# Performance work log

Hardware: AMD Instinct MI355X
Metric: run time of the kernel (lower is better)

The kernel has to match this reference:

```python
import jax, jax.numpy as jnp
import numpy as np

SEQ, B, OBS, H = 128, 256, 64, 1024

def setup_inputs() -> dict:
    key = jax.random.key(0)
    ks = jax.random.split(key, 16)
    s = 0.03  # keep weights small so tanh/sigmoid stay in a sane range
    n = lambda k, shape, sc=s: jax.random.normal(k, shape, jnp.float32) * sc
    return {
        "x": jax.random.normal(ks[0], (SEQ * B, OBS), jnp.float32),
        "done": jax.random.randint(ks[1], (SEQ * B,), 0, 2).astype(jnp.int32),
        "h0": n(ks[2], (2, B, H), 0.1),
        "c0": n(ks[3], (2, B, H), 0.1),
        "W_ih0": n(ks[4], (4 * H, OBS)),
        "W_hh0": n(ks[5], (4 * H, H)),
        "b_ih0": jnp.zeros((4 * H,), jnp.float32),
        "b_hh0": jnp.zeros((4 * H,), jnp.float32),
        "W_ih1": n(ks[6], (4 * H, H)),
        "W_hh1": n(ks[7], (4 * H, H)),
        "b_ih1": jnp.zeros((4 * H,), jnp.float32),
        "b_hh1": jnp.zeros((4 * H,), jnp.float32),
        "ln_g": jnp.ones((H,), jnp.float32),
        "ln_b": jnp.zeros((H,), jnp.float32),
        "W1": n(ks[8], (512, H)),
        "b1": jnp.zeros((512,), jnp.float32),
        "W2": n(ks[9], (128, 512)),
        "b2": jnp.zeros((128,), jnp.float32),
        "W3": n(ks[10], (64, 128)),
        "b3": jnp.zeros((64,), jnp.float32),
        "Wv": n(ks[11], (1, 64)),
        "bv": jnp.zeros((1,), jnp.float32),
    }

def _lstm_cell(xin, h, c, Wih, Whh, bih, bhh):
    # PyTorch gate order: input, forget, cell(g), output
    g = xin @ Wih.T + bih + h @ Whh.T + bhh
    i, f, gg, o = jnp.split(g, 4, axis=-1)
    c2 = jax.nn.sigmoid(f) * c + jax.nn.sigmoid(i) * jnp.tanh(gg)
    h2 = jax.nn.sigmoid(o) * jnp.tanh(c2)
    return h2, c2

def reference(x, done, h0, c0, W_ih0, W_hh0, b_ih0, b_hh0, W_ih1, W_hh1,
              b_ih1, b_hh1, ln_g, ln_b, W1, b1, W2, b2, W3, b3, Wv, bv):
    batch = h0.shape[1]
    obs = x.shape[-1]
    xs = x.reshape(-1, batch, obs)                      # (S, B, obs)
    ds = done.reshape(-1, batch).astype(x.dtype)        # (S, B)

    def step(carry, td):
        h, c = carry                                    # each (2, B, H)
        xt, dt = td
        m = (1.0 - dt)[:, None]                         # reset mask (B, 1)
        h0_, c0_ = _lstm_cell(xt, h[0] * m, c[0] * m, W_ih0, W_hh0, b_ih0, b_hh0)
        h1_, c1_ = _lstm_cell(h0_, h[1] * m, c[1] * m, W_ih1, W_hh1, b_ih1, b_hh1)
        return (jnp.stack([h0_, h1_]), jnp.stack([c0_, c1_])), h1_

    (hN, cN), hs = jax.lax.scan(step, (h0, c0), (xs, ds))
    hidden = hs.reshape(-1, hs.shape[-1])               # (S*B, H)

    # LayerNorm (eps = 1e-5, torch default)
    mu = hidden.mean(-1, keepdims=True)
    var = jnp.mean(jnp.square(hidden - mu), -1, keepdims=True)
    hn = (hidden - mu) * jax.lax.rsqrt(var + 1e-5) * ln_g + ln_b

    a = jax.nn.elu(hn @ W1.T + b1)
    a = jax.nn.elu(a @ W2.T + b2)
    a = jax.nn.elu(a @ W3.T + b3)
    value = a @ Wv.T + bv                               # (S*B, 1)
    return value, hN, cN
```

## Files before the change

### kernel.cpp

```cpp
#include <hip/hip_runtime.h>
#include <cstdint>
#include <cstddef>

typedef unsigned short u16;
typedef __attribute__((ext_vector_type(8))) short short8;
typedef __attribute__((ext_vector_type(4))) float f32x4;

#define SEQ 128
#define BATCH 256
#define HID 1024
#define LSZ 262144

#define MFMA(a,b,c) __builtin_amdgcn_mfma_f32_16x16x32_bf16((a),(b),(c),0,0,0)

#define GLDS_CG(g, l) __builtin_amdgcn_global_load_lds( \
  (__attribute__((address_space(1))) void*)(uintptr_t)(const void*)(g), \
  (__attribute__((address_space(3))) void*)(unsigned)(uintptr_t)(void*)(l), 16, 0, 17)
#define GLDS_NC(g, l) __builtin_amdgcn_global_load_lds( \
  (__attribute__((address_space(1))) void*)(uintptr_t)(const void*)(g), \
  (__attribute__((address_space(3))) void*)(unsigned)(uintptr_t)(void*)(l), 16, 0, 0)

__device__ __forceinline__ u16 f2b(float f) {
  union { float f; unsigned u; } v; v.f = f;
  unsigned r = (v.u + 0x7FFFu + ((v.u >> 16) & 1u)) >> 16;
  return (u16)r;
}
__device__ __forceinline__ float b2f(u16 h) {
  union { unsigned u; float f; } v; v.u = ((unsigned)h) << 16; return v.f;
}
__device__ __forceinline__ float sigm(float x){ return 1.f/(1.f + __expf(-x)); }
__device__ __forceinline__ float tanh_f(float x){
  x = fminf(15.f, fmaxf(-15.f, x));
  float e = __expf(2.f*x); return (e-1.f)/(e+1.f);
}
__device__ __forceinline__ float eluf(float x){ return x > 0.f ? x : expm1f(x); }

__device__ __forceinline__ void store_cg(u16* p, short8 v) {
  asm volatile("global_store_dwordx4 %0, %1, off sc0 sc1" :: "v"(p), "v"(v) : "memory");
}
__device__ __forceinline__ void wait_vm0() {
  asm volatile("s_waitcnt vmcnt(0)" ::: "memory");
}
__device__ __forceinline__ void waitgroup(int* f, int tgt) {
  if (threadIdx.x < 64) {
    int idx = threadIdx.x & 31;
    while (__hip_atomic_load(f + idx, __ATOMIC_RELAXED, __HIP_MEMORY_SCOPE_AGENT) < tgt)
      __builtin_amdgcn_s_sleep(1);
  }
  asm volatile("" ::: "memory");
  __builtin_amdgcn_s_barrier();
  __builtin_amdgcn_sched_barrier(0);
}

static const size_t OFF_W0F  = 0;
static const size_t OFF_W1F  = 8912896;
static const size_t OFF_XF   = 25690112;
static const size_t OFF_H0U  = 29884416;
static const size_t OFF_C0   = 30932992;
static const size_t OFF_C1   = 31981568;
static const size_t OFF_H1U  = 33030144;
static const size_t OFF_BS0  = 100663296;
static const size_t OFF_BS1  = 100679680;
static const size_t OFF_MU   = 100697088;
static const size_t OFF_RSTD = 100828160;
static const size_t OFF_W1LN = 100959232;
static const size_t OFF_S1   = 102007808;
static const size_t OFF_B1P  = 102009856;
static const size_t OFF_W2B  = 102011904;
static const size_t OFF_W3B  = 102142976;
static const size_t OFF_A1   = 102159360;
static const size_t OFF_A2   = 0;
static const size_t OFF_A3   = 8912896;
static const size_t OFF_H0M  = 102159360;
static const size_t OFF_H1M  = 102159360 + 1048576;

__global__ void prep_wf(const float* __restrict__ wih, const float* __restrict__ whh,
                        u16* __restrict__ out, int nkb, int kx) {
  int b = blockIdx.x; int cg = b >> 3, ct = b & 7;
  int g = ct >> 1;
  int n = nkb << 9;
  for (int e = threadIdx.x; e < n; e += 256) {
    int kb = e >> 9, r = e & 511;
    int q = r >> 7, col16 = (r >> 3) & 15, j = r & 7;
    int hl = (ct & 1) * 16 + col16;
    int gr = g * HID + cg * 32 + hl;
    int k = kb * 32 + q * 8 + j;
    float w = (k < kx) ? wih[(size_t)gr * kx + k] : whh[(size_t)gr * HID + (k - kx)];
    out[((size_t)(cg * nkb + kb) * 8 + ct) * 512 + r] = f2b(w);
  }
}

__global__ void prep_w1ln(const float* __restrict__ w1, const float* __restrict__ lng,
                          const float* __restrict__ lnb, const float* __restrict__ b1,
                          u16* __restrict__ w1ln, float* __restrict__ S1, float* __restrict__ b1p) {
  int j = blockIdx.x;
  float s = 0.f, bb = 0.f;
  for (int k = threadIdx.x; k < HID; k += 256) {
    float w = w1[(size_t)j * HID + k];
    u16 q = f2b(w * lng[k]);
    w1ln[(size_t)j * HID + k] = q;
    s += b2f(q);
    bb += w * lnb[k];
  }
  __shared__ float r1[256], r2[256];
  r1[threadIdx.x] = s; r2[threadIdx.x] = bb;
  __syncthreads();
  for (int o = 128; o > 0; o >>= 1) {
    if (threadIdx.x < (unsigned)o) { r1[threadIdx.x] += r1[threadIdx.x+o]; r2[threadIdx.x] += r2[threadIdx.x+o]; }
    __syncthreads();
  }
  if (threadIdx.x == 0) { S1[j] = r1[0]; b1p[j] = b1[j] + r2[0]; }
}

__global__ void prep_misc(const float* bih0, const float* bhh0, const float* bih1, const float* bhh1,
                          const float* x, const float* h0in, const float* c0in,
                          const float* w2, const float* w3, const int* done,
                          float* bs0, float* bs1, u16* xf, u16* h0m, u16* h1m,
                          float* c0buf, float* c1buf, u16* w2b, u16* w3b, int* flg) {
  size_t i = (size_t)blockIdx.x * blockDim.x + threadIdx.x;
  if (i < 4096) { bs0[i] = bih0[i] + bhh0[i]; return; }
  i -= 4096;
  if (i < 4096) { bs1[i] = bih1[i] + bhh1[i]; return; }
  i -= 4096;
  if (i < 2097152) {
    int o = (int)i;
    int r = o & 511, tile = o >> 9;
    int q = r >> 7, rl = (r >> 3) & 15, j = r & 7;
    int kb = tile & 1, v = tile >> 1;
    int grt = v & 15, t = v >> 4;
    int row = grt * 16 + rl, k = kb * 32 + q * 8 + j;
    xf[o] = f2b(x[((size_t)t * BATCH + row) * 64 + k]);
    return;
  }
  i -= 2097152;
  if (i < 262144) {
    int o = (int)i;
    int r = o & 511, tile = o >> 9;
    int q = r >> 7, rl = (r >> 3) & 15, j = r & 7;
    int grt = tile >> 5, kb = tile & 31;
    int row = grt * 16 + rl, h = kb * 32 + q * 8 + j;
    h0m[o] = done[row] ? (u16)0 : f2b(h0in[(size_t)row * HID + h]);
    return;
  }
  i -= 262144;
  if (i < 262144) {
    int o = (int)i;
    int r = o & 511, tile = o >> 9;
    int q = r >> 7, rl = (r >> 3) & 15, j = r & 7;
    int grt = tile >> 5, kb = tile & 31;
    int row = grt * 16 + rl, h = kb * 32 + q * 8 + j;
    h1m[o] = done[row] ? (u16)0 : f2b(h0in[LSZ + (size_t)row * HID + h]);
    return;
  }
  i -= 262144;
  if (i < LSZ) { c0buf[i] = c0in[i]; return; }
  i -= LSZ;
  if (i < LSZ) { c1buf[i] = c0in[LSZ + i]; return; }
  i -= LSZ;
  if (i < 65536) { w2b[i] = f2b(w2[i]); return; }
  i -= 65536;
  if (i < 8192) { w3b[i] = f2b(w3[i]); return; }
  i -= 8192;
  if (i < 512) { flg[i] = 0; return; }
}

__global__ __launch_bounds__(256, 2) void lstm_persist(
    const u16* __restrict__ w0f, const u16* __restrict__ w1f, const u16* __restrict__ xf,
    u16* __restrict__ h0u, u16* __restrict__ h1u,
    u16* __restrict__ h0m, u16* __restrict__ h1m,
    float* __restrict__ c0b, float* __restrict__ c1b,
    const float* __restrict__ bs0, const float* __restrict__ bs1,
    const int* __restrict__ done, int* __restrict__ flg,
    float* __restrict__ dout)
{
  const int bid = blockIdx.x;
  const int layer = bid >> 8;
  const int rg = (bid >> 5) & 7;
  const int cg = bid & 31;
  const int tid = threadIdx.x;
  const int lane = tid & 63, wv = tid >> 6;
  const int quad = lane >> 4, c16 = lane & 15;
  const int NKB = layer ? 64 : 34;
  const int NC  = layer ? 8 : 5;
  const u16* Wf = layer ? w1f : w0f;
  const float* bs = layer ? bs1 : bs0;
  float* cb = layer ? c1b : c0b;
  int* fl0 = flg;
  int* fl1 = flg + 256;
  int* myf = (layer ? fl1 : fl0) + rg * 32 + cg;
  int* g0 = fl0 + rg * 32;
  int* g1 = fl1 + rg * 32;

  __shared__ __align__(16) u16 smem[32768];
  float* gl = (float*)smem;

  const short8 z8 = {0,0,0,0,0,0,0,0};

  for (int t = 0; t < SEQ; ++t) {
    if (layer == 0) {
      if (t >= 1) waitgroup(g0, t);
    } else {
      waitgroup(g0, t + 1);
      if (t >= 1) waitgroup(g1, t);
    }

    auto issueA = [&](int p) {
      int oc = p; if (oc > NC - 1) oc = NC - 1;
      u16* lb = &smem[((unsigned)(p & 3)) * 8192];
      #pragma unroll
      for (int s = 0; s < 2; ++s) {
        int kbl = wv + s * 4;
        int kb = oc * 8 + kbl; if (kb > NKB - 1) kb = NKB - 1;
        u16* lt = lb + (unsigned)(kbl * 2) * 512;
        if (layer == 0) {
          if (kb < 2) {
            #pragma unroll
            for (int j = 0; j < 2; ++j) {
              const u16* g = xf + ((size_t)((t * 16 + rg * 2 + j) * 2 + kb)) * 512 + lane * 8;
              GLDS_NC(g, lt + j * 512);
            }
          } else {
            #pragma unroll
            for (int j = 0; j < 2; ++j) {
              const u16* g = h0m + (size_t)(t & 1) * 262144
                                 + (size_t)((rg * 2 + j) * 32 + (kb - 2)) * 512 + lane * 8;
              GLDS_CG(g, lt + j * 512);
            }
          }
        } else {
          if (kb < 32) {
            #pragma unroll
            for (int j = 0; j < 2; ++j) {
              const u16* g = h0u + (size_t)((t + 1) & 1) * 262144
                                 + (size_t)((rg * 2 + j) * 32 + kb) * 512 + lane * 8;
              GLDS_CG(g, lt + j * 512);
            }
          } else {
            #pragma unroll
            for (int j = 0; j < 2; ++j) {
              const u16* g = h1m + (size_t)(t & 1) * 262144
                                 + (size_t)((rg * 2 + j) * 32 + (kb - 32)) * 512 + lane * 8;
              GLDS_CG(g, lt + j * 512);
            }
          }
        }
      }
    };

    auto loadB = [&](int p, short8 (&vB)[8][2]) {
      int oc = p; if (oc > NC - 1) oc = NC - 1;
      #pragma unroll
      for (int kbl = 0; kbl < 8; ++kbl) {
        int kb = oc * 8 + kbl; if (kb > NKB - 1) kb = NKB - 1;
        #pragma unroll
        for (int h = 0; h < 2; ++h)
          vB[kbl][h] = *(const short8*)(Wf + ((size_t)(cg * NKB + kb) * 8 + wv * 2 + h) * 512 + lane * 8);
      }
    };

    f32x4 acc[2][2];
    #pragma unroll
    for (int a = 0; a < 2; ++a) { acc[a][0] = (f32x4){0,0,0,0}; acc[a][1] = (f32x4){0,0,0,0}; }

    auto comp = [&](int p, short8 (&vB)[8][2]) {
      int kbc = NKB - p * 8; if (kbc > 8) kbc = 8;
      const u16* sb = &smem[((unsigned)(p & 3)) * 8192] + lane * 8;
      #pragma unroll
      for (int kbl = 0; kbl < 8; ++kbl) if (kbl < kbc) {
        #pragma unroll
        for (int a = 0; a < 2; ++a) {
          short8 af = *(const short8*)(sb + (kbl * 2 + a) * 512);
          acc[a][0] = MFMA(af, vB[kbl][0], acc[a][0]);
          acc[a][1] = MFMA(af, vB[kbl][1], acc[a][1]);
        }
      }
    };

    short8 vB0[8][2], vB1[8][2];

    loadB(0, vB0);
    asm volatile("" ::: "memory");
    issueA(0);
    asm volatile("" ::: "memory");
    issueA(1);

#define CHUNK(CC, VBL, VBU) \
    loadB((CC) + 1, VBL); \
    asm volatile("" ::: "memory"); \
    issueA((CC) + 2); \
    asm volatile("s_waitcnt vmcnt(24)" ::: "memory"); \
    __builtin_amdgcn_s_barrier(); \
    __builtin_amdgcn_sched_barrier(0); \
    comp((CC), VBU);

    int c = 0;
    for (;;) {
      CHUNK(c, vB1, vB0) if (++c == NC) break;
      CHUNK(c, vB0, vB1) if (++c == NC) break;
    }
#undef CHUNK

    wait_vm0();
    __syncthreads();

    #pragma unroll
    for (int a = 0; a < 2; ++a)
      #pragma unroll
      for (int ct = 0; ct < 2; ++ct)
        #pragma unroll
        for (int rgi = 0; rgi < 4; ++rgi)
          gl[(a * 16 + quad * 4 + rgi) * 132 + wv * 32 + ct * 16 + c16] = acc[a][ct][rgi];
    __syncthreads();

    if (layer == 0 && t >= 2) waitgroup(g1, t - 1);

    if (tid < 128) {
      int row = tid >> 2;
      int q = tid & 3;
      int h8 = q * 8;
      int rowg = rg * 32 + row;
      int H0 = cg * 32 + h8;
      const float* glp = gl + row * 132;
      float m = done[t * BATCH + rowg] ? 0.f : 1.f;
      int nx = (t < SEQ - 1) ? done[(t + 1) * BATCH + rowg] : 0;
      float* cp = cb + (size_t)rowg * HID + H0;
      short8 hv;
      float h2a[8], c2a[8];
      #pragma unroll
      for (int j = 0; j < 8; ++j) {
        float ivv = glp[h8 + j]      + bs[H0 + j];
        float fvv = glp[32 + h8 + j] + bs[HID + H0 + j];
        float gvv = glp[64 + h8 + j] + bs[2*HID + H0 + j];
        float ovv = glp[96 + h8 + j] + bs[3*HID + H0 + j];
        float c2 = sigm(fvv) * (cp[j] * m) + sigm(ivv) * tanh_f(gvv);
        float h2 = sigm(ovv) * tanh_f(c2);
        cp[j] = c2;
        h2a[j] = h2; c2a[j] = c2;
        ((u16*)&hv)[j] = f2b(h2);
      }
      short8 hm = nx ? z8 : hv;
      size_t off = (size_t)((rg * 2 + (row >> 4)) * 32 + cg) * 512 + (size_t)(q * 16 + (row & 15)) * 8;
      if (layer == 0) {
        store_cg(h0u + (size_t)((t + 1) & 1) * 262144 + off, hv);
        if (t < SEQ - 1) store_cg(h0m + (size_t)((t + 1) & 1) * 262144 + off, hm);
      } else {
        store_cg(h1u + (size_t)(t + 1) * 262144 + off, hv);
        if (t < SEQ - 1) store_cg(h1m + (size_t)((t + 1) & 1) * 262144 + off, hm);
      }
      if (t == SEQ - 1) {
        float* dh = dout + 32768 + (size_t)layer * LSZ + (size_t)rowg * HID + H0;
        float* dc = dout + 32768 + 2 * LSZ + (size_t)layer * LSZ + (size_t)rowg * HID + H0;
        #pragma unroll
        for (int j = 0; j < 8; ++j) { dh[j] = h2a[j]; dc[j] = c2a[j]; }
      }
    }
    wait_vm0();
    __syncthreads();
    if (tid == 0) __hip_atomic_fetch_add(myf, 1, __ATOMIC_RELAXED, __HIP_MEMORY_SCOPE_AGENT);
  }
}

__global__ void ln_stats(const u16* __restrict__ h1u, float* __restrict__ mu, float* __restrict__ rstd) {
  int R = blockIdx.x * 4 + (threadIdx.x >> 6);
  int l = threadIdx.x & 63;
  int t = R >> 8, brow = R & 255, grt = brow >> 4, rl = brow & 15;
  const u16* base = h1u + (size_t)(t + 1) * 262144 + (size_t)(grt * 32 + (l >> 1)) * 512;
  int q2 = (l & 1) * 2;
  short8 v0 = *(const short8*)(base + (q2 * 16 + rl) * 8);
  short8 v1 = *(const short8*)(base + ((q2 + 1) * 16 + rl) * 8);
  float s = 0.f, q = 0.f;
  #pragma unroll
  for (int e = 0; e < 8; ++e) {
    float a = b2f((u16)v0[e]); s += a; q += a*a;
    float b = b2f((u16)v1[e]); s += b; q += b*b;
  }
  for (int o = 32; o > 0; o >>= 1) { s += __shfl_xor(s, o); q += __shfl_xor(q, o); }
  if (l == 0) {
    float mm = s * (1.f/1024.f);
    float var = q * (1.f/1024.f) - mm*mm;
    mu[R] = mm; rstd[R] = rsqrtf(var + 1e-5f);
  }
}

__global__ __launch_bounds__(512, 4) void mlp_gemm(
    const u16* __restrict__ A, int lda, int amode,
    const u16* __restrict__ B, int K, int N,
    u16* __restrict__ out, int ldo, int mode, int swiz,
    const float* __restrict__ mu, const float* __restrict__ rstd,
    const float* __restrict__ S1v, const float* __restrict__ bias)
{
  int nt, mtb;
  if (swiz) { int p = blockIdx.x * gridDim.y + blockIdx.y; nt = p & 3; mtb = p >> 2; }
  else { nt = blockIdx.x; mtb = blockIdx.y; }
  const int tid = threadIdx.x, lane = tid & 63, wv = tid >> 6;
  const int quad = lane >> 4, c16 = lane & 15;
  __shared__ __align__(16) u16 Am[16384], Bm[16384];
  f32x4 acc[8];
  #pragma unroll
  for (int i = 0; i < 8; ++i) acc[i] = (f32x4){0.f,0.f,0.f,0.f};

  int arow[4], akl[4], bcol[4];
  #pragma unroll
  for (int i = 0; i < 4; ++i) {
    int s = tid + i * 512, sub = s >> 6, lp = s & 63;
    int ks = sub >> 3, u = sub & 7;
    arow[i] = mtb * 128 + u * 16 + (lp & 15);
    akl[i]  = ks * 32 + (lp >> 4) * 8;
    bcol[i] = nt * 128 + u * 16 + (lp & 15);
  }
  short8 vA[4], vB[4];
  const short8 z8 = {0,0,0,0,0,0,0,0};
  const int NCH = K >> 7;
  auto load_stage = [&](int ci) {
    int kc = ci << 7;
    #pragma unroll
    for (int i = 0; i < 4; ++i) {
      if (amode) {
        int R = arow[i], k = kc + akl[i];
        const u16* p = A + (size_t)((R >> 8) + 1) * 262144
                         + (size_t)(((R >> 4) & 15) * 32 + (k >> 5)) * 512
                         + (size_t)((((k >> 3) & 3) * 16 + (R & 15)) * 8);
        vA[i] = *(const short8*)p;
      } else {
        vA[i] = *(const short8*)(A + (size_t)arow[i] * lda + kc + akl[i]);
      }
      vB[i] = (bcol[i] < N) ? *(const short8*)(B + (size_t)bcol[i] * K + kc + akl[i]) : z8;
    }
  };
  load_stage(0);
  for (int ci = 0; ci < NCH; ++ci) {
    #pragma unroll
    for (int i = 0; i < 4; ++i) {
      *(short8*)&Am[(size_t)(tid + i*512) * 8] = vA[i];
      *(short8*)&Bm[(size_t)(tid + i*512) * 8] = vB[i];
    }
    __syncthreads();
    if (ci + 1 < NCH) load_stage(ci + 1);
    #pragma unroll
    for (int ks = 0; ks < 4; ++ks) {
      short8 bf = *(const short8*)&Bm[((ks*8 + wv)*64 + lane) * 8];
      #pragma unroll
      for (int rt = 0; rt < 8; ++rt) {
        short8 af = *(const short8*)&Am[((ks*8 + rt)*64 + lane) * 8];
        acc[rt] = MFMA(af, bf, acc[rt]);
      }
    }
    __syncthreads();
  }
  int col = nt * 128 + wv * 16 + c16;
  if (col < N) {
    #pragma unroll
    for (int rt = 0; rt < 8; ++rt) {
      #pragma unroll
      for (int rgi = 0; rgi < 4; ++rgi) {
        int row = mtb * 128 + rt * 16 + quad * 4 + rgi;
        float v = acc[rt][rgi];
        if (mode == 0) v = v * rstd[row] - mu[row] * rstd[row] * S1v[col] + bias[col];
        else           v = v + bias[col];
        v = eluf(v);
        out[(size_t)row * ldo + col] = f2b(v);
      }
    }
  }
}

__global__ void value_head(const u16* __restrict__ a3, const float* __restrict__ wv,
                           const float* __restrict__ bv, float* __restrict__ dout) {
  int row = blockIdx.x * 256 + threadIdx.x;
  const short8* p = (const short8*)(a3 + (size_t)row * 64);
  float s = bv[0];
  #pragma unroll
  for (int j = 0; j < 8; ++j) {
    short8 v = p[j];
    #pragma unroll
    for (int e = 0; e < 8; ++e) s += b2f((u16)v[e]) * wv[j*8+e];
  }
  dout[row] = s;
}

extern "C" void kernel_launch(void* const* d_in, const int* in_sizes, int n_in,
                              void* d_out, int out_size, void* d_ws, size_t ws_size,
                              hipStream_t stream) {
  (void)in_sizes; (void)n_in; (void)out_size; (void)ws_size;
  const float* x    = (const float*)d_in[0];
  const int*   done = (const int*)d_in[1];
  const float* h0in = (const float*)d_in[2];
  const float* c0in = (const float*)d_in[3];
  const float* wih0 = (const float*)d_in[4];
  const float* whh0 = (const float*)d_in[5];
  const float* bih0 = (const float*)d_in[6];
  const float* bhh0 = (const float*)d_in[7];
  const float* wih1 = (const float*)d_in[8];
  const float* whh1 = (const float*)d_in[9];
  const float* bih1 = (const float*)d_in[10];
  const float* bhh1 = (const float*)d_in[11];
  const float* lng  = (const float*)d_in[12];
  const float* lnb  = (const float*)d_in[13];
  const float* w1   = (const float*)d_in[14];
  const float* b1   = (const float*)d_in[15];
  const float* w2   = (const float*)d_in[16];
  const float* b2   = (const float*)d_in[17];
  const float* w3   = (const float*)d_in[18];
  const float* b3   = (const float*)d_in[19];
  const float* wvp  = (const float*)d_in[20];
  const float* bvp  = (const float*)d_in[21];
  float* dout = (float*)d_out;
  char* ws = (char*)d_ws;

  u16*   w0f  = (u16*)(ws + OFF_W0F);
  u16*   w1f  = (u16*)(ws + OFF_W1F);
  u16*   xf   = (u16*)(ws + OFF_XF);
  u16*   h0u  = (u16*)(ws + OFF_H0U);
  u16*   h1u  = (u16*)(ws + OFF_H1U);
  u16*   h0m  = (u16*)(ws + OFF_H0M);
  u16*   h1m  = (u16*)(ws + OFF_H1M);
  float* c0b  = (float*)(ws + OFF_C0);
  float* c1b  = (float*)(ws + OFF_C1);
  float* bs0  = (float*)(ws + OFF_BS0);
  float* bs1  = (float*)(ws + OFF_BS1);
  int*   flg  = (int*)(ws + OFF_MU);
  float* mu   = (float*)(ws + OFF_MU);
  float* rstd = (float*)(ws + OFF_RSTD);
  u16*   w1ln = (u16*)(ws + OFF_W1LN);
  float* s1   = (float*)(ws + OFF_S1);
  float* b1p  = (float*)(ws + OFF_B1P);
  u16*   w2b  = (u16*)(ws + OFF_W2B);
  u16*   w3b  = (u16*)(ws + OFF_W3B);
  u16*   a1   = (u16*)(ws + OFF_A1);
  u16*   a2   = (u16*)(ws + OFF_A2);
  u16*   a3   = (u16*)(ws + OFF_A3);

  prep_wf<<<256, 256, 0, stream>>>(wih0, whh0, w0f, 34, 64);
  prep_wf<<<256, 256, 0, stream>>>(wih1, whh1, w1f, 64, 1024);
  prep_w1ln<<<512, 256, 0, stream>>>(w1, lng, lnb, b1, w1ln, s1, b1p);
  prep_misc<<<12610, 256, 0, stream>>>(bih0, bhh0, bih1, bhh1, x, h0in, c0in, w2, w3, done,
                                       bs0, bs1, xf, h0m, h1m, c0b, c1b, w2b, w3b, flg);

  lstm_persist<<<512, 256, 0, stream>>>(w0f, w1f, xf, h0u, h1u, h0m, h1m, c0b, c1b,
                                        bs0, bs1, done, flg, dout);

  ln_stats<<<8192, 256, 0, stream>>>(h1u, mu, rstd);
  mlp_gemm<<<dim3(8, 128), 512, 0, stream>>>(h1u, 0, 1, w1ln, 1024, 512, a1, 512, 0, 1, mu, rstd, s1, b1p);
  mlp_gemm<<<dim3(1, 256), 512, 0, stream>>>(a1, 512, 0, w2b, 512, 128, a2, 128, 1, 0, mu, rstd, s1, b2);
  mlp_gemm<<<dim3(1, 256), 512, 0, stream>>>(a2, 128, 0, w3b, 128, 64, a3, 64, 1, 0, mu, rstd, s1, b3);
  value_head<<<128, 256, 0, stream>>>(a3, wvp, bvp, dout);
}
```

Measured before the change: 2.730 ms.

## Use per-timestep hidden-state buffers to drop WAR wait and cache-bypass loads

When the workspace is large enough, the hidden-state exchange buffers (h0u, h1m, h0m) are indexed by timestep instead of double-buffered by parity. Because each slot is written only once, layer 0 no longer has to wait for layer 1 to finish reading before overwriting, and the readers can use normal cached loads instead of system-coherent ones. The cost is a much larger workspace footprint, with tiered fallbacks to the old scheme. Relying on ordinary cached loads across blocks assumes stale lines for those fresh addresses are never present in cache.

Result: no change. 2.769 ms (+1.4%).

```diff
diff --git a/kernel.cpp b/kernel.cpp
--- a/kernel.cpp
+++ b/kernel.cpp
@@ -13,7 +13,7 @@
 
 #define MFMA(a,b,c) __builtin_amdgcn_mfma_f32_16x16x32_bf16((a),(b),(c),0,0,0)
 
-#define GLDS_CG(g, l) __builtin_amdgcn_global_load_lds( \
+#define GLDS_SC(g, l) __builtin_amdgcn_global_load_lds( \
   (__attribute__((address_space(1))) void*)(uintptr_t)(const void*)(g), \
   (__attribute__((address_space(3))) void*)(unsigned)(uintptr_t)(void*)(l), 16, 0, 17)
 #define GLDS_NC(g, l) __builtin_amdgcn_global_load_lds( \
@@ -55,7 +55,6 @@
 static const size_t OFF_W0F  = 0;
 static const size_t OFF_W1F  = 8912896;
 static const size_t OFF_XF   = 25690112;
-static const size_t OFF_H0U  = 29884416;
 static const size_t OFF_C0   = 30932992;
 static const size_t OFF_C1   = 31981568;
 static const size_t OFF_H1U  = 33030144;
@@ -71,8 +70,15 @@
 static const size_t OFF_A1   = 102159360;
 static const size_t OFF_A2   = 0;
 static const size_t OFF_A3   = 8912896;
-static const size_t OFF_H0M  = 102159360;
-static const size_t OFF_H1M  = 102159360 + 1048576;
+static const size_t OFF_H0M_R  = 102159360;
+static const size_t OFF_H1M_R  = 103207936;
+static const size_t OFF_H0U_R  = 104256512;
+static const size_t OFF_H0U_PT = 106353664;
+static const size_t OFF_H1M_PT = 173986816;
+static const size_t OFF_H0M_PT = 241095680;
+static const size_t NEED1 = 173986816;
+static const size_t NEED2 = 241095680;
+static const size_t NEED3 = 308204544;
 
 __global__ void prep_wf(const float* __restrict__ wih, const float* __restrict__ whh,
                         u16* __restrict__ out, int nkb, int kx) {
@@ -171,7 +177,7 @@
     float* __restrict__ c0b, float* __restrict__ c1b,
     const float* __restrict__ bs0, const float* __restrict__ bs1,
     const int* __restrict__ done, int* __restrict__ flg,
-    float* __restrict__ dout)
+    float* __restrict__ dout, int tier)
 {
   const int bid = blockIdx.x;
   const int layer = bid >> 8;
@@ -204,6 +210,10 @@
       if (t >= 1) waitgroup(g1, t);
     }
 
+    const size_t s_h0m = (size_t)(tier >= 3 ? (unsigned)t : (unsigned)(t & 1)) * 262144;
+    const size_t s_h0u = (size_t)(tier >= 1 ? (unsigned)(t + 1) : (unsigned)((t + 1) & 1)) * 262144;
+    const size_t s_h1m = (size_t)(tier >= 2 ? (unsigned)t : (unsigned)(t & 1)) * 262144;
+
     auto issueA = [&](int p) {
       int oc = p; if (oc > NC - 1) oc = NC - 1;
       u16* lb = &smem[((unsigned)(p & 3)) * 8192];
@@ -222,25 +232,22 @@
           } else {
             #pragma unroll
             for (int j = 0; j < 2; ++j) {
-              const u16* g = h0m + (size_t)(t & 1) * 262144
-                                 + (size_t)((rg * 2 + j) * 32 + (kb - 2)) * 512 + lane * 8;
-              GLDS_CG(g, lt + j * 512);
+              const u16* g = h0m + s_h0m + (size_t)((rg * 2 + j) * 32 + (kb - 2)) * 512 + lane * 8;
+              if (tier >= 3) { GLDS_NC(g, lt + j * 512); } else { GLDS_SC(g, lt + j * 512); }
             }
           }
         } else {
           if (kb < 32) {
             #pragma unroll
             for (int j = 0; j < 2; ++j) {
-              const u16* g = h0u + (size_t)((t + 1) & 1) * 262144
-                                 + (size_t)((rg * 2 + j) * 32 + kb) * 512 + lane * 8;
-              GLDS_CG(g, lt + j * 512);
+              const u16* g = h0u + s_h0u + (size_t)((rg * 2 + j) * 32 + kb) * 512 + lane * 8;
+              if (tier >= 1) { GLDS_NC(g, lt + j * 512); } else { GLDS_SC(g, lt + j * 512); }
             }
           } else {
             #pragma unroll
             for (int j = 0; j < 2; ++j) {
-              const u16* g = h1m + (size_t)(t & 1) * 262144
-                                 + (size_t)((rg * 2 + j) * 32 + (kb - 32)) * 512 + lane * 8;
-              GLDS_CG(g, lt + j * 512);
+              const u16* g = h1m + s_h1m + (size_t)((rg * 2 + j) * 32 + (kb - 32)) * 512 + lane * 8;
+              if (tier >= 2) { GLDS_NC(g, lt + j * 512); } else { GLDS_SC(g, lt + j * 512); }
             }
           }
         }
@@ -312,7 +319,7 @@
           gl[(a * 16 + quad * 4 + rgi) * 132 + wv * 32 + ct * 16 + c16] = acc[a][ct][rgi];
     __syncthreads();
 
-    if (layer == 0 && t >= 2) waitgroup(g1, t - 1);
+    if (layer == 0 && tier < 1 && t >= 2) waitgroup(g1, t - 1);
 
     if (tid < 128) {
       int row = tid >> 2;
@@ -340,12 +347,15 @@
       }
       short8 hm = nx ? z8 : hv;
       size_t off = (size_t)((rg * 2 + (row >> 4)) * 32 + cg) * 512 + (size_t)(q * 16 + (row & 15)) * 8;
+      size_t w_h0u = (size_t)(tier >= 1 ? (unsigned)(t + 1) : (unsigned)((t + 1) & 1)) * 262144;
+      size_t w_h0m = (size_t)(tier >= 3 ? (unsigned)(t + 1) : (unsigned)((t + 1) & 1)) * 262144;
+      size_t w_h1m = (size_t)(tier >= 2 ? (unsigned)(t + 1) : (unsigned)((t + 1) & 1)) * 262144;
       if (layer == 0) {
-        store_cg(h0u + (size_t)((t + 1) & 1) * 262144 + off, hv);
-        if (t < SEQ - 1) store_cg(h0m + (size_t)((t + 1) & 1) * 262144 + off, hm);
+        store_cg(h0u + w_h0u + off, hv);
+        if (t < SEQ - 1) store_cg(h0m + w_h0m + off, hm);
       } else {
         store_cg(h1u + (size_t)(t + 1) * 262144 + off, hv);
-        if (t < SEQ - 1) store_cg(h1m + (size_t)((t + 1) & 1) * 262144 + off, hm);
+        if (t < SEQ - 1) store_cg(h1m + w_h1m + off, hm);
       }
       if (t == SEQ - 1) {
         float* dh = dout + 32768 + (size_t)layer * LSZ + (size_t)rowg * HID + H0;
@@ -481,7 +491,7 @@
 extern "C" void kernel_launch(void* const* d_in, const int* in_sizes, int n_in,
                               void* d_out, int out_size, void* d_ws, size_t ws_size,
                               hipStream_t stream) {
-  (void)in_sizes; (void)n_in; (void)out_size; (void)ws_size;
+  (void)in_sizes; (void)n_in; (void)out_size;
   const float* x    = (const float*)d_in[0];
   const int*   done = (const int*)d_in[1];
   const float* h0in = (const float*)d_in[2];
@@ -507,13 +517,18 @@
   float* dout = (float*)d_out;
   char* ws = (char*)d_ws;
 
+  int tier = 0;
+  if (ws_size >= NEED3)      tier = 3;
+  else if (ws_size >= NEED2) tier = 2;
+  else if (ws_size >= NEED1) tier = 1;
+
   u16*   w0f  = (u16*)(ws + OFF_W0F);
   u16*   w1f  = (u16*)(ws + OFF_W1F);
   u16*   xf   = (u16*)(ws + OFF_XF);
-  u16*   h0u  = (u16*)(ws + OFF_H0U);
   u16*   h1u  = (u16*)(ws + OFF_H1U);
-  u16*   h0m  = (u16*)(ws + OFF_H0M);
-  u16*   h1m  = (u16*)(ws + OFF_H1M);
+  u16*   h0u  = (u16*)(ws + (tier >= 1 ? OFF_H0U_PT : OFF_H0U_R));
+  u16*   h1m  = (u16*)(ws + (tier >= 2 ? OFF_H1M_PT : OFF_H1M_R));
+  u16*   h0m  = (u16*)(ws + (tier >= 3 ? OFF_H0M_PT : OFF_H0M_R));
   float* c0b  = (float*)(ws + OFF_C0);
   float* c1b  = (float*)(ws + OFF_C1);
   float* bs0  = (float*)(ws + OFF_BS0);
@@ -537,7 +552,7 @@
                                        bs0, bs1, xf, h0m, h1m, c0b, c1b, w2b, w3b, flg);
 
   lstm_persist<<<512, 256, 0, stream>>>(w0f, w1f, xf, h0u, h1u, h0m, h1m, c0b, c1b,
-                                        bs0, bs1, done, flg, dout);
+                                        bs0, bs1, done, flg, dout, tier);
 
   ln_stats<<<8192, 256, 0, stream>>>(h1u, mu, rstd);
   mlp_gemm<<<dim3(8, 128), 512, 0, stream>>>(h1u, 0, 1, w1ln, 1024, 512, a1, 512, 0, 1, mu, rstd, s1, b1p);
```
